# Kernel optimization log

Hardware: AMD Instinct MI355X
Metric: run time of the kernel (lower is better)

The kernel has to match this reference:

```python
import jax, jax.numpy as jnp
import numpy as np

N_NODES = 100000
N_EDGES = 1600000
N_PAIRS = 500000
K_HOPS = 6


def _bn(x, g, b, eps):
    # training-mode batch norm over the node/edge (batch) axis, biased variance
    mu = jnp.mean(x, axis=0)
    var = jnp.var(x, axis=0)
    return (x - mu) * jax.lax.rsqrt(var + eps) * g + b


def _gelu(x):
    return jax.nn.gelu(x, approximate=False)  # torch GELU default (erf)


def setup_inputs() -> dict:
    key = jax.random.key(0)
    ks = jax.random.split(key, 20)
    F, EF = 128, 32

    def w(k, shape, s=0.05):
        return jax.random.normal(k, shape, dtype=jnp.float32) * s

    return {
        'X': jax.random.normal(ks[0], (N_NODES, F), jnp.float32),
        'Y': jax.random.normal(ks[1], (N_PAIRS, EF), jnp.float32),
        'edge_index': jax.random.randint(ks[2], (2, N_EDGES), 0, N_NODES, jnp.int32),
        'inds0': jax.random.randint(ks[3], (N_PAIRS,), 0, N_NODES, jnp.int32),
        'inds1': jax.random.randint(ks[4], (N_PAIRS,), 0, N_NODES, jnp.int32),
        'bn_node_g': jnp.ones((F,), jnp.float32),
        'bn_node_b': jnp.zeros((F,), jnp.float32),
        'tag_lin_W': w(ks[5], (F, 128)),
        'tag_lin_b': jnp.zeros((128,), jnp.float32),
        'tag_Ws': w(ks[6], (K_HOPS + 1, 128, 128)),
        'tag_bias': jnp.zeros((128,), jnp.float32),
        'nl_W0': w(ks[7], (256, 256)),
        'nl_b0': jnp.zeros((256,), jnp.float32),
        'nl_W1': w(ks[8], (256, 128)),
        'nl_b1': jnp.zeros((128,), jnp.float32),
        'cl_W': w(ks[9], (128, 128)),
        'cl_b': jnp.zeros((128,), jnp.float32),
        'end_W': w(ks[10], (128, 8)),
        'end_b': jnp.zeros((8,), jnp.float32),
        'bn_edge_g': jnp.ones((544,), jnp.float32),
        'bn_edge_b': jnp.zeros((544,), jnp.float32),
        'el_W0': w(ks[11], (544, 512)),
        'el_b0': jnp.zeros((512,), jnp.float32),
        'el_W1': w(ks[12], (512, 256)),
        'el_b1': jnp.zeros((256,), jnp.float32),
        'el_end_W': w(ks[13], (256, 1)),
        'el_end_b': jnp.zeros((1,), jnp.float32),
    }


def reference(X, Y, bn_node_g, bn_node_b, tag_lin_W, tag_lin_b, tag_Ws, tag_bias,
              nl_W0, nl_b0, nl_W1, nl_b1, cl_W, cl_b, end_W, end_b,
              bn_edge_g, bn_edge_b, el_W0, el_b0, el_W1, el_b1, el_end_W, el_end_b,
              edge_index, inds0, inds1):
    N = X.shape[0]
    # ---- NodeGLAM ----
    x = _bn(X, bn_node_g, bn_node_b, 1e-5)
    # TagModule: Linear -> GELU -> TAGConv -> GELU
    h = _gelu(x @ tag_lin_W + tag_lin_b)
    src, dst = edge_index[0], edge_index[1]
    # gcn_norm (no self loops): deg over target, norm = d^-1/2[src]*d^-1/2[dst]
    deg = jax.ops.segment_sum(jnp.ones(src.shape, h.dtype), dst, num_segments=N)
    dinv = jnp.where(deg > 0, jax.lax.rsqrt(jnp.maximum(deg, 1.0)), 0.0)
    wgt = (dinv[src] * dinv[dst])[:, None]  # [E,1]
    out = h @ tag_Ws[0]
    hk = h
    for k in range(1, K_HOPS + 1):
        hk = jax.ops.segment_sum(hk[src] * wgt, dst, num_segments=N)  # gather-scale-scatter
        out = out + hk @ tag_Ws[k]
    h = _gelu(out + tag_bias)
    a = jnp.concatenate([x, h], axis=1)  # [N, 256]
    a = _gelu(a @ nl_W0 + nl_b0)
    a = _gelu(a @ nl_W1 + nl_b1)  # Node_embs [N,128]
    cl = _gelu(a @ cl_W + cl_b)
    node_classes = jax.nn.softmax(cl @ end_W + end_b, axis=-1)  # [N,8]
    # ---- edge feature gather + EdgeGLAM ----
    Omega = jnp.concatenate([a[inds0], a[inds1], X[inds0], X[inds1], Y], axis=1)  # [P,544]
    o = _bn(Omega, bn_edge_g, bn_edge_b, 1.0)  # BatchNorm(input_, output_) -> eps=1
    o = _gelu(o @ el_W0 + el_b0)
    o = _gelu(o @ el_W1 + el_b1)
    e_pred = jax.nn.sigmoid(o @ el_end_W + el_end_b)[:, 0]  # [P]
    return (node_classes, e_pred)
```

## Files before the change

kernel.cpp:

```cpp
#include <hip/hip_runtime.h>
#include <math.h>

#define NN 100000
#define NE 1600000
#define NP 500000
#define KHOPS 6
#define ECHK 50000
#define NB_SCAN ((NN + 1023) / 1024)

typedef unsigned short u16;
typedef short bf16x8 __attribute__((ext_vector_type(8)));
typedef float f32x4 __attribute__((ext_vector_type(4)));

__device__ __forceinline__ float gelu_erf(float x) {
    return 0.5f * x * (1.0f + erff(x * 0.70710678118654752f));
}
__device__ __forceinline__ float b2f(u16 u) {
    return __uint_as_float(((unsigned int)u) << 16);
}
__device__ __forceinline__ u16 f2b(float f) {
    unsigned int x = __float_as_uint(f);
    return (u16)((x + 0x7FFFu + ((x >> 16) & 1u)) >> 16);
}
__device__ __forceinline__ bf16x8 cvt8(float4 a, float4 b) {
    bf16x8 v;
    v[0]=(short)f2b(a.x); v[1]=(short)f2b(a.y); v[2]=(short)f2b(a.z); v[3]=(short)f2b(a.w);
    v[4]=(short)f2b(b.x); v[5]=(short)f2b(b.y); v[6]=(short)f2b(b.z); v[7]=(short)f2b(b.w);
    return v;
}

template<int BF>
__global__ void col_stats(const void* __restrict__ Matv, int rows, int lc,
                          const int* __restrict__ w0, const int* __restrict__ w1,
                          float* __restrict__ sums, float* __restrict__ sumsq,
                          int base0, int base1)
{
    __shared__ float red[256];
    const int t = threadIdx.x;
    const int C = 1 << lc;
    const long total = (long)rows << lc;
    const long stride = (long)gridDim.x * 256;
    float s0 = 0.f, q0 = 0.f, s1 = 0.f, q1 = 0.f;
    for (long idx = (long)blockIdx.x * 256 + t; idx < total; idx += stride) {
        int r = (int)(idx >> lc);
        float v = BF ? b2f(((const u16*)Matv)[idx]) : ((const float*)Matv)[idx];
        float f0 = w0 ? (float)w0[r] : 1.0f;
        s0 += f0 * v;
        q0 += f0 * v * v;
        if (w1) {
            float f1 = (float)w1[r];
            s1 += f1 * v;
            q1 += f1 * v * v;
        }
    }
    red[t] = s0; __syncthreads();
    if (t < C) { float x = 0.f; for (int k = t; k < 256; k += C) x += red[k]; atomicAdd(&sums[base0 + t], x); }
    __syncthreads();
    red[t] = q0; __syncthreads();
    if (t < C) { float x = 0.f; for (int k = t; k < 256; k += C) x += red[k]; atomicAdd(&sumsq[base0 + t], x); }
    __syncthreads();
    if (w1) {
        red[t] = s1; __syncthreads();
        if (t < C) { float x = 0.f; for (int k = t; k < 256; k += C) x += red[k]; atomicAdd(&sums[base1 + t], x); }
        __syncthreads();
        red[t] = q1; __syncthreads();
        if (t < C) { float x = 0.f; for (int k = t; k < 256; k += C) x += red[k]; atomicAdd(&sumsq[base1 + t], x); }
    }
}

__global__ void bn_finalize(const float* __restrict__ sums, const float* __restrict__ sumsq,
                            const float* __restrict__ g, const float* __restrict__ b,
                            float* __restrict__ s, float* __restrict__ t,
                            int C, float count, float eps)
{
    int c = blockIdx.x * blockDim.x + threadIdx.x;
    if (c < C) {
        float mu = sums[c] / count;
        float var = sumsq[c] / count - mu * mu;
        float sc = g[c] * rsqrtf(var + eps);
        s[c] = sc;
        t[c] = b[c] - mu * sc;
    }
}

__global__ void hist_add(const int* __restrict__ idx, int n, int* __restrict__ cnt)
{
    int stride = gridDim.x * blockDim.x;
    for (int i = blockIdx.x * blockDim.x + threadIdx.x; i < n; i += stride)
        atomicAdd(&cnt[idx[i]], 1);
}

__global__ void hist_add2(const int* __restrict__ i0, const int* __restrict__ i1, int n,
                          int* __restrict__ c0, int* __restrict__ c1)
{
    int stride = gridDim.x * blockDim.x;
    for (int i = blockIdx.x * blockDim.x + threadIdx.x; i < n; i += stride) {
        atomicAdd(&c0[i0[i]], 1);
        atomicAdd(&c1[i1[i]], 1);
    }
}

__global__ void scan1(const int* __restrict__ cnt, int* __restrict__ ex,
                      int* __restrict__ part, int n)
{
    __shared__ int buf[1024];
    int b = blockIdx.x, t = threadIdx.x;
    int i = b * 1024 + t;
    int v = (i < n) ? cnt[i] : 0;
    buf[t] = v;
    __syncthreads();
    int incl = v;
    for (int o = 1; o < 1024; o <<= 1) {
        int tmp = (t >= o) ? buf[t - o] : 0;
        __syncthreads();
        incl += tmp;
        buf[t] = incl;
        __syncthreads();
    }
    if (i < n) ex[i] = incl - v;
    if (t == 1023) part[b] = incl;
}

__global__ void scan2(int* __restrict__ part, int nb)
{
    __shared__ int s[256];
    int t = threadIdx.x;
    if (t < nb) s[t] = part[t];
    __syncthreads();
    if (t == 0) {
        int run = 0;
        for (int b = 0; b < nb; ++b) { int x = s[b]; part[b] = run; run += x; }
        part[nb] = run;
    }
}

__global__ void scan3(int* __restrict__ indptr, const int* __restrict__ part,
                      const int* __restrict__ cnt, float* __restrict__ dinv, int n)
{
    int b = blockIdx.x, t = threadIdx.x;
    int i = b * 1024 + t;
    if (i < n) {
        indptr[i] += part[b];
        int c = cnt[i];
        dinv[i] = (c > 0) ? rsqrtf((float)c) : 0.f;
    }
    if (b == 0 && t == 0) indptr[n] = part[NB_SCAN];
}

__global__ void csr_build(const int* __restrict__ src, const int* __restrict__ dst, int n,
                          const int* __restrict__ indptr, int* __restrict__ cursor,
                          int* __restrict__ csrS)
{
    int stride = gridDim.x * blockDim.x;
    for (int e = blockIdx.x * blockDim.x + threadIdx.x; e < n; e += stride) {
        int s = src[e], d = dst[e];
        int pos = indptr[d] + atomicAdd(&cursor[d], 1);
        csrS[pos] = s;
    }
}

__global__ void spmm_hop(const u16* __restrict__ hin, u16* __restrict__ hout,
                         const int* __restrict__ indptr, const int* __restrict__ csrS,
                         const float* __restrict__ dinv)
{
    int gid = blockIdx.x * blockDim.x + threadIdx.x;
    int node = gid >> 6;
    int lane = gid & 63;
    if (node >= NN) return;
    float dn = dinv[node];
    int beg = indptr[node], end = indptr[node + 1];
    float a0 = 0.f, a1 = 0.f;
    int e = beg;
    for (; e + 3 < end; e += 4) {
        int s0 = csrS[e], s1 = csrS[e + 1], s2 = csrS[e + 2], s3 = csrS[e + 3];
        float w0 = dn * dinv[s0], w1 = dn * dinv[s1];
        float w2 = dn * dinv[s2], w3 = dn * dinv[s3];
        ushort2 p0 = *(const ushort2*)(hin + (size_t)s0 * 128 + lane * 2);
        ushort2 p1 = *(const ushort2*)(hin + (size_t)s1 * 128 + lane * 2);
        ushort2 p2 = *(const ushort2*)(hin + (size_t)s2 * 128 + lane * 2);
        ushort2 p3 = *(const ushort2*)(hin + (size_t)s3 * 128 + lane * 2);
        a0 = fmaf(w0, b2f(p0.x), a0); a1 = fmaf(w0, b2f(p0.y), a1);
        a0 = fmaf(w1, b2f(p1.x), a0); a1 = fmaf(w1, b2f(p1.y), a1);
        a0 = fmaf(w2, b2f(p2.x), a0); a1 = fmaf(w2, b2f(p2.y), a1);
        a0 = fmaf(w3, b2f(p3.x), a0); a1 = fmaf(w3, b2f(p3.y), a1);
    }
    for (; e < end; ++e) {
        int s0 = csrS[e];
        float w0 = dn * dinv[s0];
        ushort2 p0 = *(const ushort2*)(hin + (size_t)s0 * 128 + lane * 2);
        a0 = fmaf(w0, b2f(p0.x), a0);
        a1 = fmaf(w0, b2f(p0.y), a1);
    }
    ushort2 o;
    o.x = f2b(a0); o.y = f2b(a1);
    *(ushort2*)(hout + (size_t)node * 128 + lane * 2) = o;
}

__global__ void convTB(const float* __restrict__ in, u16* __restrict__ out,
                       int K, int Nc, int B)
{
    int per = K * Nc;
    int i = blockIdx.x * blockDim.x + threadIdx.x;
    if (i < per * B) {
        int m = i / per, r = i - m * per;
        int n = r / K, k = r - n * K;
        out[i] = f2b(in[(size_t)m * per + (size_t)k * Nc + n]);
    }
}

__global__ void convB(const float* __restrict__ in, u16* __restrict__ out, int n4)
{
    int stride = gridDim.x * blockDim.x;
    for (int i = blockIdx.x * blockDim.x + threadIdx.x; i < n4; i += stride) {
        float4 v = ((const float4*)in)[i];
        ushort4 o;
        o.x = f2b(v.x); o.y = f2b(v.y); o.z = f2b(v.z); o.w = f2b(v.w);
        ((ushort4*)out)[i] = o;
    }
}

__global__ void fold_wT(const float* __restrict__ W0, const float* __restrict__ s,
                        u16* __restrict__ out)
{
    int i = blockIdx.x * blockDim.x + threadIdx.x;
    if (i < 512 * 544) {
        int n = i / 544, k = i - n * 544;
        out[i] = f2b(s[k] * W0[(size_t)k * 512 + n]);
    }
}

__global__ void fold_b(const float* __restrict__ W0, const float* __restrict__ b0,
                       const float* __restrict__ tv, float* __restrict__ bp)
{
    int j = blockIdx.x * blockDim.x + threadIdx.x;
    if (j < 512) {
        float s = b0[j];
        for (int k = 0; k < 544; ++k) s = fmaf(tv[k], W0[k * 512 + j], s);
        bp[j] = s;
    }
}

template<int AMODE>
__device__ __forceinline__ bf16x8 load_a_slot(
    const void* __restrict__ A0v, const void* __restrict__ A1v,
    const float* __restrict__ Yp, const int* __restrict__ i0s, const int* __restrict__ i1s,
    int rowOffset, const float* __restrict__ sv, const float* __restrict__ tv,
    int row, int r, int k0, int sl, int Mr, int lda)
{
    bf16x8 val = {0, 0, 0, 0, 0, 0, 0, 0};
    if (row < Mr) {
        if (AMODE == 0) {
            val = *(const bf16x8*)((const u16*)A0v + (size_t)row * lda + k0 + sl * 8);
        } else if (AMODE == 1) {
            int c = k0 + sl * 8;
            if (c < 128) {
                const float* xp = (const float*)A0v + (size_t)row * 128 + c;
                float4 x0 = *(const float4*)xp, x1 = *(const float4*)(xp + 4);
                float4 s0 = *(const float4*)(sv + c), s1 = *(const float4*)(sv + c + 4);
                float4 t0 = *(const float4*)(tv + c), t1 = *(const float4*)(tv + c + 4);
                float4 a = make_float4(fmaf(x0.x,s0.x,t0.x), fmaf(x0.y,s0.y,t0.y),
                                       fmaf(x0.z,s0.z,t0.z), fmaf(x0.w,s0.w,t0.w));
                float4 b = make_float4(fmaf(x1.x,s1.x,t1.x), fmaf(x1.y,s1.y,t1.y),
                                       fmaf(x1.z,s1.z,t1.z), fmaf(x1.w,s1.w,t1.w));
                val = cvt8(a, b);
            } else {
                val = *(const bf16x8*)((const u16*)A1v + (size_t)row * 128 + (c - 128));
            }
        } else if (AMODE == 3) {
            int c = k0 + sl * 8;
            const float* xp = (const float*)A0v + (size_t)row * 128 + c;
            float4 x0 = *(const float4*)xp, x1 = *(const float4*)(xp + 4);
            float4 s0 = *(const float4*)(sv + c), s1 = *(const float4*)(sv + c + 4);
            float4 t0 = *(const float4*)(tv + c), t1 = *(const float4*)(tv + c + 4);
            float4 a = make_float4(fmaf(x0.x,s0.x,t0.x), fmaf(x0.y,s0.y,t0.y),
                                   fmaf(x0.z,s0.z,t0.z), fmaf(x0.w,s0.w,t0.w));
            float4 b = make_float4(fmaf(x1.x,s1.x,t1.x), fmaf(x1.y,s1.y,t1.y),
                                   fmaf(x1.z,s1.z,t1.z), fmaf(x1.w,s1.w,t1.w));
            val = cvt8(a, b);
        } else {
            int seg = k0 >> 7;
            int c = (k0 & 127) + sl * 8;
            if (seg == 0) {
                val = *(const bf16x8*)((const u16*)A0v + (size_t)i0s[r] * 128 + c);
            } else if (seg == 1) {
                val = *(const bf16x8*)((const u16*)A0v + (size_t)i1s[r] * 128 + c);
            } else if (seg == 2) {
                val = *(const bf16x8*)((const u16*)A1v + (size_t)i0s[r] * 128 + c);
            } else if (seg == 3) {
                val = *(const bf16x8*)((const u16*)A1v + (size_t)i1s[r] * 128 + c);
            } else {
                const float* yp = Yp + (size_t)(rowOffset + row) * 32 + sl * 8;
                val = cvt8(*(const float4*)yp, *(const float4*)(yp + 4));
            }
        }
    }
    return val;
}

template<int AMODE, int ACT, int ACCUM, int OUTBF>
__launch_bounds__(256, 2)
__global__ void gemm_mfma(const void* __restrict__ A0v, const void* __restrict__ A1v,
                          const float* __restrict__ Yp,
                          const int* __restrict__ I0, const int* __restrict__ I1,
                          int rowOffset,
                          const float* __restrict__ sv, const float* __restrict__ tv,
                          const u16* __restrict__ Wb, const float* __restrict__ bias,
                          void* __restrict__ Cv, const float* __restrict__ Cacc,
                          int Mr, int Kd, int Nc, int lda)
{
    __shared__ __align__(16) u16 As[128 * 32];
    __shared__ __align__(16) u16 Bs[128 * 32];
    __shared__ int i0s[128], i1s[128];

    const int t = threadIdx.x;
    const int lane = t & 63;
    const int wid = t >> 6;
    const int wm = wid >> 1, wn = wid & 1;
    const int lb = lane & 15, lh = lane >> 4;
    const int row0 = blockIdx.x * 128;
    const int colb = blockIdx.y * 128;

    if (AMODE == 2) {
        if (t < 128) {
            int r = row0 + t;
            i0s[t] = (r < Mr) ? I0[rowOffset + r] : 0;
        } else {
            int r = row0 + (t - 128);
            i1s[t - 128] = (r < Mr) ? I1[rowOffset + r] : 0;
        }
    }

    f32x4 acc[4][4];
#pragma unroll
    for (int i = 0; i < 4; ++i)
#pragma unroll
        for (int j = 0; j < 4; ++j) acc[i][j] = (f32x4){0.f, 0.f, 0.f, 0.f};

    for (int k0 = 0; k0 < Kd; k0 += 32) {
        __syncthreads();
#pragma unroll
        for (int h = 0; h < 2; ++h) {
            int s = t + h * 256;
            int r = s >> 2, sl = s & 3;
            bf16x8 val = load_a_slot<AMODE>(A0v, A1v, Yp, i0s, i1s, rowOffset, sv, tv,
                                            row0 + r, r, k0, sl, Mr, lda);
            *(bf16x8*)&As[r * 32 + ((sl ^ ((r >> 1) & 3)) << 3)] = val;
        }
#pragma unroll
        for (int h = 0; h < 2; ++h) {
            int s = t + h * 256;
            int n = s >> 2, sl = s & 3;
            bf16x8 val = *(const bf16x8*)(Wb + (size_t)(colb + n) * Kd + k0 + sl * 8);
            *(bf16x8*)&Bs[n * 32 + ((sl ^ ((n >> 1) & 3)) << 3)] = val;
        }
        __syncthreads();
        bf16x8 af[4], bfr[4];
#pragma unroll
        for (int i = 0; i < 4; ++i) {
            int r = wm * 64 + i * 16 + lb;
            af[i] = *(const bf16x8*)&As[r * 32 + ((lh ^ ((r >> 1) & 3)) << 3)];
        }
#pragma unroll
        for (int j = 0; j < 4; ++j) {
            int n = wn * 64 + j * 16 + lb;
            bfr[j] = *(const bf16x8*)&Bs[n * 32 + ((lh ^ ((n >> 1) & 3)) << 3)];
        }
#pragma unroll
        for (int i = 0; i < 4; ++i)
#pragma unroll
            for (int j = 0; j < 4; ++j)
                acc[i][j] = __builtin_amdgcn_mfma_f32_16x16x32_bf16(af[i], bfr[j], acc[i][j], 0, 0, 0);
    }

#pragma unroll
    for (int i = 0; i < 4; ++i) {
#pragma unroll
        for (int j = 0; j < 4; ++j) {
            int col = colb + wn * 64 + j * 16 + lb;
#pragma unroll
            for (int r = 0; r < 4; ++r) {
                int row = row0 + wm * 64 + i * 16 + lh * 4 + r;
                if (row < Mr) {
                    size_t off = (size_t)row * Nc + col;
                    float v = acc[i][j][r];
                    if (ACCUM) v += Cacc[off];
                    if (ACT) v = gelu_erf(v + bias[col]);
                    if (OUTBF) ((u16*)Cv)[off] = f2b(v);
                    else       ((float*)Cv)[off] = v;
                }
            }
        }
    }
}

template<int AMODE, int ACT, int OUTBF>
__launch_bounds__(512, 4)
__global__ void gemm_wide(const void* __restrict__ A0v, const void* __restrict__ A1v,
                          const float* __restrict__ Yp,
                          const int* __restrict__ I0, const int* __restrict__ I1,
                          int rowOffset,
                          const float* __restrict__ sv, const float* __restrict__ tv,
                          const u16* __restrict__ Wb, const float* __restrict__ bias,
                          void* __restrict__ Cv, int Mr, int Kd, int Nc)
{
    __shared__ __align__(16) u16 As[128 * 32];
    __shared__ __align__(16) u16 Bs[256 * 32];
    __shared__ int i0s[128], i1s[128];

    const int t = threadIdx.x;
    const int lane = t & 63;
    const int wid = t >> 6;
    const int wm = wid >> 2, wn = wid & 3;
    const int lb = lane & 15, lh = lane >> 4;
    const int row0 = blockIdx.x * 128;
    const int colb = blockIdx.y * 256;

    if (AMODE == 2) {
        if (t < 128) {
            int r = row0 + t;
            i0s[t] = (r < Mr) ? I0[rowOffset + r] : 0;
        } else if (t < 256) {
            int r = row0 + (t - 128);
            i1s[t - 128] = (r < Mr) ? I1[rowOffset + r] : 0;
        }
    }

    f32x4 acc[4][4];
#pragma unroll
    for (int i = 0; i < 4; ++i)
#pragma unroll
        for (int j = 0; j < 4; ++j) acc[i][j] = (f32x4){0.f, 0.f, 0.f, 0.f};

    for (int k0 = 0; k0 < Kd; k0 += 32) {
        __syncthreads();
        {
            int r = t >> 2, sl = t & 3;
            bf16x8 val = load_a_slot<AMODE>(A0v, A1v, Yp, i0s, i1s, rowOffset, sv, tv,
                                            row0 + r, r, k0, sl, Mr, 0);
            *(bf16x8*)&As[r * 32 + ((sl ^ ((r >> 1) & 3)) << 3)] = val;
        }
#pragma unroll
        for (int h = 0; h < 2; ++h) {
            int s = t + h * 512;
            int n = s >> 2, sl = s & 3;
            bf16x8 val = *(const bf16x8*)(Wb + (size_t)(colb + n) * Kd + k0 + sl * 8);
            *(bf16x8*)&Bs[n * 32 + ((sl ^ ((n >> 1) & 3)) << 3)] = val;
        }
        __syncthreads();
        bf16x8 af[4], bfr[4];
#pragma unroll
        for (int i = 0; i < 4; ++i) {
            int r = wm * 64 + i * 16 + lb;
            af[i] = *(const bf16x8*)&As[r * 32 + ((lh ^ ((r >> 1) & 3)) << 3)];
        }
#pragma unroll
        for (int j = 0; j < 4; ++j) {
            int n = wn * 64 + j * 16 + lb;
            bfr[j] = *(const bf16x8*)&Bs[n * 32 + ((lh ^ ((n >> 1) & 3)) << 3)];
        }
#pragma unroll
        for (int i = 0; i < 4; ++i)
#pragma unroll
            for (int j = 0; j < 4; ++j)
                acc[i][j] = __builtin_amdgcn_mfma_f32_16x16x32_bf16(af[i], bfr[j], acc[i][j], 0, 0, 0);
    }

#pragma unroll
    for (int i = 0; i < 4; ++i) {
#pragma unroll
        for (int j = 0; j < 4; ++j) {
            int col = colb + wn * 64 + j * 16 + lb;
#pragma unroll
            for (int r = 0; r < 4; ++r) {
                int row = row0 + wm * 64 + i * 16 + lh * 4 + r;
                if (row < Mr) {
                    size_t off = (size_t)row * Nc + col;
                    float v = acc[i][j][r];
                    if (ACT) v = gelu_erf(v + bias[col]);
                    if (OUTBF) ((u16*)Cv)[off] = f2b(v);
                    else       ((float*)Cv)[off] = v;
                }
            }
        }
    }
}

__launch_bounds__(512, 4)
__global__ void gemm_head(const u16* __restrict__ A0, const u16* __restrict__ Wb,
                          const float* __restrict__ bias, const float* __restrict__ eW,
                          const float* __restrict__ eb,
                          float* __restrict__ outp, int outOffset, int Mr)
{
    __shared__ __align__(16) u16 As[128 * 32];
    __shared__ __align__(16) u16 Bs[256 * 32];
    __shared__ float bls[256], ews[256];
    __shared__ float sred[4][128];

    const int t = threadIdx.x;
    const int lane = t & 63;
    const int wid = t >> 6;
    const int wm = wid >> 2, wn = wid & 3;
    const int lb = lane & 15, lh = lane >> 4;
    const int row0 = blockIdx.x * 128;
    const int Kd = 512;

    if (t < 256) { bls[t] = bias[t]; ews[t] = eW[t]; }

    f32x4 acc[4][4];
#pragma unroll
    for (int i = 0; i < 4; ++i)
#pragma unroll
        for (int j = 0; j < 4; ++j) acc[i][j] = (f32x4){0.f, 0.f, 0.f, 0.f};

    for (int k0 = 0; k0 < Kd; k0 += 32) {
        __syncthreads();
        {
            int r = t >> 2, sl = t & 3;
            int row = row0 + r;
            bf16x8 val = {0,0,0,0,0,0,0,0};
            if (row < Mr) val = *(const bf16x8*)(A0 + (size_t)row * 512 + k0 + sl * 8);
            *(bf16x8*)&As[r * 32 + ((sl ^ ((r >> 1) & 3)) << 3)] = val;
        }
#pragma unroll
        for (int h = 0; h < 2; ++h) {
            int s = t + h * 512;
            int n = s >> 2, sl = s & 3;
            bf16x8 val = *(const bf16x8*)(Wb + (size_t)n * Kd + k0 + sl * 8);
            *(bf16x8*)&Bs[n * 32 + ((sl ^ ((n >> 1) & 3)) << 3)] = val;
        }
        __syncthreads();
        bf16x8 af[4], bfr[4];
#pragma unroll
        for (int i = 0; i < 4; ++i) {
            int r = wm * 64 + i * 16 + lb;
            af[i] = *(const bf16x8*)&As[r * 32 + ((lh ^ ((r >> 1) & 3)) << 3)];
        }
#pragma unroll
        for (int j = 0; j < 4; ++j) {
            int n = wn * 64 + j * 16 + lb;
            bfr[j] = *(const bf16x8*)&Bs[n * 32 + ((lh ^ ((n >> 1) & 3)) << 3)];
        }
#pragma unroll
        for (int i = 0; i < 4; ++i)
#pragma unroll
            for (int j = 0; j < 4; ++j)
                acc[i][j] = __builtin_amdgcn_mfma_f32_16x16x32_bf16(af[i], bfr[j], acc[i][j], 0, 0, 0);
    }

#pragma unroll
    for (int i = 0; i < 4; ++i) {
#pragma unroll
        for (int r = 0; r < 4; ++r) {
            float p = 0.f;
#pragma unroll
            for (int j = 0; j < 4; ++j) {
                int col = wn * 64 + j * 16 + lb;
                p += gelu_erf(acc[i][j][r] + bls[col]) * ews[col];
            }
            p += __shfl_xor(p, 1);
            p += __shfl_xor(p, 2);
            p += __shfl_xor(p, 4);
            p += __shfl_xor(p, 8);
            if (lb == 0) sred[wn][wm * 64 + i * 16 + lh * 4 + r] = p;
        }
    }
    __syncthreads();
    if (t < 128) {
        int row = row0 + t;
        if (row < Mr) {
            float s = sred[0][t] + sred[1][t] + sred[2][t] + sred[3][t] + eb[0];
            outp[outOffset + row] = 1.f / (1.f + expf(-s));
        }
    }
}

__global__ void node_head(const float* __restrict__ cl, const float* __restrict__ Wend,
                          const float* __restrict__ bend, float* __restrict__ out, int m)
{
    __shared__ float WsT[8 * 128];
    __shared__ float bs[8];
    int t = threadIdx.x;
    for (int i = t; i < 1024; i += 256) {
        int k = i >> 3, j = i & 7;
        WsT[j * 128 + k] = Wend[i];
    }
    if (t < 8) bs[t] = bend[t];
    __syncthreads();
    int gid = blockIdx.x * 256 + t;
    int wave = gid >> 6, lane = gid & 63;
    if (wave >= m) return;
    float v0 = cl[(size_t)wave * 128 + lane];
    float v1 = cl[(size_t)wave * 128 + lane + 64];
    float lg[8];
#pragma unroll
    for (int j = 0; j < 8; ++j) {
        float p = v0 * WsT[j * 128 + lane] + v1 * WsT[j * 128 + lane + 64];
#pragma unroll
        for (int o = 32; o; o >>= 1) p += __shfl_down(p, o);
        lg[j] = p;
    }
    if (lane == 0) {
        float mx = -1e30f;
#pragma unroll
        for (int j = 0; j < 8; ++j) { lg[j] += bs[j]; mx = fmaxf(mx, lg[j]); }
        float s = 0.f;
#pragma unroll
        for (int j = 0; j < 8; ++j) { lg[j] = expf(lg[j] - mx); s += lg[j]; }
        float inv = 1.f / s;
#pragma unroll
        for (int j = 0; j < 8; ++j) out[(size_t)wave * 8 + j] = lg[j] * inv;
    }
}

extern "C" void kernel_launch(void* const* d_in, const int* in_sizes, int n_in,
                              void* d_out, int out_size, void* d_ws, size_t ws_size,
                              hipStream_t stream)
{
    const float* X    = (const float*)d_in[0];
    const float* Y    = (const float*)d_in[1];
    const int*   EI   = (const int*)d_in[2];
    const int*   I0   = (const int*)d_in[3];
    const int*   I1   = (const int*)d_in[4];
    const float* bnG  = (const float*)d_in[5];
    const float* bnB  = (const float*)d_in[6];
    const float* Wlin = (const float*)d_in[7];
    const float* blin = (const float*)d_in[8];
    const float* tagWs= (const float*)d_in[9];
    const float* tagB = (const float*)d_in[10];
    const float* nlW0 = (const float*)d_in[11];
    const float* nlb0 = (const float*)d_in[12];
    const float* nlW1 = (const float*)d_in[13];
    const float* nlb1 = (const float*)d_in[14];
    const float* clW  = (const float*)d_in[15];
    const float* clb  = (const float*)d_in[16];
    const float* endW = (const float*)d_in[17];
    const float* endB = (const float*)d_in[18];
    const float* beG  = (const float*)d_in[19];
    const float* beB  = (const float*)d_in[20];
    const float* elW0 = (const float*)d_in[21];
    const float* elb0 = (const float*)d_in[22];
    const float* elW1 = (const float*)d_in[23];
    const float* elb1 = (const float*)d_in[24];
    const float* elEW = (const float*)d_in[25];
    const float* elEb = (const float*)d_in[26];

    const int N = NN, E = NE, P = NP;

    char* w = (char*)d_ws;
    size_t off = 0;
    auto alloc = [&](size_t bytes) -> void* {
        void* p = w + off;
        off += (bytes + 255) & ~(size_t)255;
        return p;
    };

    size_t zeroBytes = (size_t)(544 + 544 + 128 + 128) * 4 + (size_t)4 * N * 4;
    char* zr = (char*)alloc(zeroBytes);
    float* statS = (float*)zr;
    float* statQ = statS + 544;
    float* nodeS = statQ + 544;
    float* nodeQ = nodeS + 128;
    int* cnt    = (int*)(nodeQ + 128);
    int* cursor = cnt + N;
    int* cnt0   = cursor + N;
    int* cnt1   = cnt0 + N;

    int*   indptr = (int*)alloc((size_t)(N + 1) * 4);
    int*   part   = (int*)alloc((size_t)(NB_SCAN + 1) * 4);
    float* dinv   = (float*)alloc((size_t)N * 4);
    int*   csrS   = (int*)alloc((size_t)E * 4);
    float* sNode  = (float*)alloc(128 * 4);
    float* tNode  = (float*)alloc(128 * 4);
    float* sEdge  = (float*)alloc(544 * 4);
    float* tEdge  = (float*)alloc(544 * 4);
    float* b0p    = (float*)alloc(512 * 4);
    u16* Wlinb  = (u16*)alloc((size_t)128 * 128 * 2);
    u16* tagWsb = (u16*)alloc((size_t)7 * 128 * 128 * 2);
    u16* nlW0b  = (u16*)alloc((size_t)256 * 256 * 2);
    u16* nlW1b  = (u16*)alloc((size_t)128 * 256 * 2);
    u16* clWb   = (u16*)alloc((size_t)128 * 128 * 2);
    u16* elW1b  = (u16*)alloc((size_t)256 * 512 * 2);
    u16* W0pb   = (u16*)alloc((size_t)512 * 544 * 2);
    u16*   hA   = (u16*)alloc((size_t)N * 128 * 2);
    u16*   hB   = (u16*)alloc((size_t)N * 128 * 2);
    float* outT = (float*)alloc((size_t)N * 128 * 4);

    if (ws_size < off) return;

    u16*   aEmb  = hA;
    u16*   houtb = hB;
    float* out_nodes = (float*)d_out;
    float* out_epred = (float*)d_out + (size_t)N * 8;

    hipMemsetAsync(zr, 0, zeroBytes, stream);

    convTB<<<(128*128 + 255)/256, 256, 0, stream>>>(Wlin, Wlinb, 128, 128, 1);
    convTB<<<(7*128*128 + 255)/256, 256, 0, stream>>>(tagWs, tagWsb, 128, 128, 7);
    convTB<<<(256*256 + 255)/256, 256, 0, stream>>>(nlW0, nlW0b, 256, 256, 1);
    convTB<<<(256*128 + 255)/256, 256, 0, stream>>>(nlW1, nlW1b, 256, 128, 1);
    convTB<<<(128*128 + 255)/256, 256, 0, stream>>>(clW, clWb, 128, 128, 1);
    convTB<<<(512*256 + 255)/256, 256, 0, stream>>>(elW1, elW1b, 512, 256, 1);

    col_stats<0><<<1024, 256, 0, stream>>>(X, N, 7, nullptr, nullptr, nodeS, nodeQ, 0, 0);
    bn_finalize<<<1, 128, 0, stream>>>(nodeS, nodeQ, bnG, bnB, sNode, tNode, 128, (float)N, 1e-5f);

    dim3 g1((N + 127) / 128, 1);
    gemm_mfma<3, 1, 0, 1><<<g1, 256, 0, stream>>>(X, nullptr, nullptr, nullptr, nullptr, 0,
                                                  sNode, tNode, Wlinb, blin, hA, nullptr, N, 128, 128, 128);

    hist_add<<<2048, 256, 0, stream>>>(EI + E, E, cnt);
    hist_add2<<<1024, 256, 0, stream>>>(I0, I1, P, cnt0, cnt1);
    scan1<<<NB_SCAN, 1024, 0, stream>>>(cnt, indptr, part, N);
    scan2<<<1, 256, 0, stream>>>(part, NB_SCAN);
    scan3<<<NB_SCAN, 1024, 0, stream>>>(indptr, part, cnt, dinv, N);
    csr_build<<<2048, 256, 0, stream>>>(EI, EI + E, E, indptr, cursor, csrS);

    gemm_mfma<0, 0, 0, 0><<<g1, 256, 0, stream>>>(hA, nullptr, nullptr, nullptr, nullptr, 0,
                                                  nullptr, nullptr, tagWsb, nullptr, outT, nullptr,
                                                  N, 128, 128, 128);
    u16* cur = hA; u16* nxt = hB;
    for (int k = 1; k < KHOPS; ++k) {
        spmm_hop<<<(N * 64 + 255) / 256, 256, 0, stream>>>(cur, nxt, indptr, csrS, dinv);
        gemm_mfma<0, 0, 1, 0><<<g1, 256, 0, stream>>>(nxt, nullptr, nullptr, nullptr, nullptr, 0,
                                                      nullptr, nullptr, tagWsb + (size_t)k*128*128,
                                                      nullptr, outT, outT, N, 128, 128, 128);
        u16* tmp = cur; cur = nxt; nxt = tmp;
    }
    spmm_hop<<<(N * 64 + 255) / 256, 256, 0, stream>>>(cur, nxt, indptr, csrS, dinv);
    gemm_mfma<0, 1, 1, 1><<<g1, 256, 0, stream>>>(nxt, nullptr, nullptr, nullptr, nullptr, 0,
                                                  nullptr, nullptr, tagWsb + (size_t)KHOPS*128*128,
                                                  tagB, houtb, outT, N, 128, 128, 128);

    u16*   a256  = (u16*)outT;
    float* clbuf = outT;
    {
        dim3 gA((N + 127) / 128, 1);
        gemm_wide<1, 1, 1><<<gA, 512, 0, stream>>>(X, houtb, nullptr, nullptr, nullptr, 0,
                                                   sNode, tNode, nlW0b, nlb0, a256, N, 256, 256);
        dim3 gB((N + 127) / 128, 1);
        gemm_mfma<0, 1, 0, 1><<<gB, 256, 0, stream>>>(a256, nullptr, nullptr, nullptr, nullptr, 0,
                                                      nullptr, nullptr, nlW1b, nlb1, aEmb, nullptr,
                                                      N, 256, 128, 256);
        gemm_mfma<0, 1, 0, 0><<<gB, 256, 0, stream>>>(aEmb, nullptr, nullptr, nullptr, nullptr, 0,
                                                      nullptr, nullptr, clWb, clb, clbuf, nullptr,
                                                      N, 128, 128, 128);
        node_head<<<(N + 3) / 4, 256, 0, stream>>>(clbuf, endW, endB, out_nodes, N);
    }

    u16* Xb = hB;
    convB<<<2048, 256, 0, stream>>>(X, Xb, N * 128 / 4);

    col_stats<1><<<1024, 256, 0, stream>>>(aEmb, N, 7, cnt0, cnt1, statS, statQ, 0, 128);
    col_stats<1><<<1024, 256, 0, stream>>>(Xb,   N, 7, cnt0, cnt1, statS, statQ, 256, 384);
    col_stats<0><<<1024, 256, 0, stream>>>(Y,    P, 5, nullptr, nullptr, statS, statQ, 512, 0);
    bn_finalize<<<3, 256, 0, stream>>>(statS, statQ, beG, beB, sEdge, tEdge, 544, (float)P, 1.0f);
    fold_wT<<<(512*544 + 255)/256, 256, 0, stream>>>(elW0, sEdge, W0pb);
    fold_b<<<2, 256, 0, stream>>>(elW0, elb0, tEdge, b0p);

    u16* o1 = (u16*)outT;
    for (int pb = 0; pb < P; pb += ECHK) {
        int m = (P - pb < ECHK) ? (P - pb) : ECHK;
        dim3 gA((m + 127) / 128, 2);
        gemm_wide<2, 1, 1><<<gA, 512, 0, stream>>>(aEmb, Xb, Y, I0, I1, pb,
                                                   nullptr, nullptr, W0pb, b0p, o1, m, 544, 512);
        dim3 gB((m + 127) / 128, 1);
        gemm_head<<<gB, 512, 0, stream>>>(o1, elW1b, elb1, elEW, elEb, out_epred, pb, m);
    }
}
```

Baseline: 2.339 ms.

## Pair TAG hop GEMMs, unroll SpMM gather by 8, widen edge GEMM tile

New measurement: 4.848 ms. 2.07x slower.

```diff
diff --git a/kernel.cpp b/kernel.cpp
--- a/kernel.cpp
+++ b/kernel.cpp
@@ -171,18 +171,20 @@
     int beg = indptr[node], end = indptr[node + 1];
     float a0 = 0.f, a1 = 0.f;
     int e = beg;
-    for (; e + 3 < end; e += 4) {
-        int s0 = csrS[e], s1 = csrS[e + 1], s2 = csrS[e + 2], s3 = csrS[e + 3];
-        float w0 = dn * dinv[s0], w1 = dn * dinv[s1];
-        float w2 = dn * dinv[s2], w3 = dn * dinv[s3];
-        ushort2 p0 = *(const ushort2*)(hin + (size_t)s0 * 128 + lane * 2);
-        ushort2 p1 = *(const ushort2*)(hin + (size_t)s1 * 128 + lane * 2);
-        ushort2 p2 = *(const ushort2*)(hin + (size_t)s2 * 128 + lane * 2);
-        ushort2 p3 = *(const ushort2*)(hin + (size_t)s3 * 128 + lane * 2);
-        a0 = fmaf(w0, b2f(p0.x), a0); a1 = fmaf(w0, b2f(p0.y), a1);
-        a0 = fmaf(w1, b2f(p1.x), a0); a1 = fmaf(w1, b2f(p1.y), a1);
-        a0 = fmaf(w2, b2f(p2.x), a0); a1 = fmaf(w2, b2f(p2.y), a1);
-        a0 = fmaf(w3, b2f(p3.x), a0); a1 = fmaf(w3, b2f(p3.y), a1);
+    for (; e + 7 < end; e += 8) {
+        int sidx[8];
+        ushort2 pv[8];
+#pragma unroll
+        for (int u = 0; u < 8; ++u) sidx[u] = csrS[e + u];
+#pragma unroll
+        for (int u = 0; u < 8; ++u)
+            pv[u] = *(const ushort2*)(hin + (size_t)sidx[u] * 128 + lane * 2);
+#pragma unroll
+        for (int u = 0; u < 8; ++u) {
+            float wv = dn * dinv[sidx[u]];
+            a0 = fmaf(wv, b2f(pv[u].x), a0);
+            a1 = fmaf(wv, b2f(pv[u].y), a1);
+        }
     }
     for (; e < end; ++e) {
         int s0 = csrS[e];
@@ -208,6 +210,18 @@
     }
 }
 
+__global__ void conv_pair(const float* __restrict__ Ws, u16* __restrict__ out)
+{
+    int i = blockIdx.x * blockDim.x + threadIdx.x;
+    if (i < 3 * 128 * 256) {
+        int p = i >> 15;
+        int r = i & 32767;
+        int n = r >> 8, k = r & 255;
+        int hop = 2 * p + (k >> 7);
+        out[i] = f2b(Ws[(size_t)hop * 16384 + (size_t)(k & 127) * 128 + n]);
+    }
+}
+
 __global__ void convB(const float* __restrict__ in, u16* __restrict__ out, int n4)
 {
     int stride = gridDim.x * blockDim.x;
@@ -251,6 +265,10 @@
     if (row < Mr) {
         if (AMODE == 0) {
             val = *(const bf16x8*)((const u16*)A0v + (size_t)row * lda + k0 + sl * 8);
+        } else if (AMODE == 5) {
+            int c = k0 + sl * 8;
+            const u16* Ap = (c < 128) ? (const u16*)A0v : (const u16*)A1v;
+            val = *(const bf16x8*)(Ap + (size_t)row * 128 + (c & 127));
         } else if (AMODE == 1) {
             int c = k0 + sl * 8;
             if (c < 128) {
@@ -393,7 +411,7 @@
     }
 }
 
-template<int AMODE, int ACT, int OUTBF>
+template<int AMODE, int ACT, int OUTBF, int NCOLS>
 __launch_bounds__(512, 4)
 __global__ void gemm_wide(const void* __restrict__ A0v, const void* __restrict__ A1v,
                           const float* __restrict__ Yp,
@@ -403,8 +421,12 @@
                           const u16* __restrict__ Wb, const float* __restrict__ bias,
                           void* __restrict__ Cv, int Mr, int Kd, int Nc)
 {
+    constexpr int NJ = NCOLS / 64;
+    constexpr int WCOL = NCOLS / 4;
+    constexpr int BH = NCOLS / 128;
+
     __shared__ __align__(16) u16 As[128 * 32];
-    __shared__ __align__(16) u16 Bs[256 * 32];
+    __shared__ __align__(16) u16 Bs[NCOLS * 32];
     __shared__ int i0s[128], i1s[128];
 
     const int t = threadIdx.x;
@@ -413,7 +435,7 @@
     const int wm = wid >> 2, wn = wid & 3;
     const int lb = lane & 15, lh = lane >> 4;
     const int row0 = blockIdx.x * 128;
-    const int colb = blockIdx.y * 256;
+    const int colb = blockIdx.y * NCOLS;
 
     if (AMODE == 2) {
         if (t < 128) {
@@ -425,11 +447,11 @@
         }
     }
 
-    f32x4 acc[4][4];
+    f32x4 acc[4][NJ];
 #pragma unroll
     for (int i = 0; i < 4; ++i)
 #pragma unroll
-        for (int j = 0; j < 4; ++j) acc[i][j] = (f32x4){0.f, 0.f, 0.f, 0.f};
+        for (int j = 0; j < NJ; ++j) acc[i][j] = (f32x4){0.f, 0.f, 0.f, 0.f};
 
     for (int k0 = 0; k0 < Kd; k0 += 32) {
         __syncthreads();
@@ -440,36 +462,36 @@
             *(bf16x8*)&As[r * 32 + ((sl ^ ((r >> 1) & 3)) << 3)] = val;
         }
 #pragma unroll
-        for (int h = 0; h < 2; ++h) {
+        for (int h = 0; h < BH; ++h) {
             int s = t + h * 512;
             int n = s >> 2, sl = s & 3;
             bf16x8 val = *(const bf16x8*)(Wb + (size_t)(colb + n) * Kd + k0 + sl * 8);
             *(bf16x8*)&Bs[n * 32 + ((sl ^ ((n >> 1) & 3)) << 3)] = val;
         }
         __syncthreads();
-        bf16x8 af[4], bfr[4];
+        bf16x8 af[4], bfr[NJ];
 #pragma unroll
         for (int i = 0; i < 4; ++i) {
             int r = wm * 64 + i * 16 + lb;
             af[i] = *(const bf16x8*)&As[r * 32 + ((lh ^ ((r >> 1) & 3)) << 3)];
         }
 #pragma unroll
-        for (int j = 0; j < 4; ++j) {
-            int n = wn * 64 + j * 16 + lb;
+        for (int j = 0; j < NJ; ++j) {
+            int n = wn * WCOL + j * 16 + lb;
             bfr[j] = *(const bf16x8*)&Bs[n * 32 + ((lh ^ ((n >> 1) & 3)) << 3)];
         }
 #pragma unroll
         for (int i = 0; i < 4; ++i)
 #pragma unroll
-            for (int j = 0; j < 4; ++j)
+            for (int j = 0; j < NJ; ++j)
                 acc[i][j] = __builtin_amdgcn_mfma_f32_16x16x32_bf16(af[i], bfr[j], acc[i][j], 0, 0, 0);
     }
 
 #pragma unroll
     for (int i = 0; i < 4; ++i) {
 #pragma unroll
-        for (int j = 0; j < 4; ++j) {
-            int col = colb + wn * 64 + j * 16 + lb;
+        for (int j = 0; j < NJ; ++j) {
+            int col = colb + wn * WCOL + j * 16 + lb;
 #pragma unroll
             for (int r = 0; r < 4; ++r) {
                 int row = row0 + wm * 64 + i * 16 + lh * 4 + r;
@@ -675,7 +697,8 @@
     float* tEdge  = (float*)alloc(544 * 4);
     float* b0p    = (float*)alloc(512 * 4);
     u16* Wlinb  = (u16*)alloc((size_t)128 * 128 * 2);
-    u16* tagWsb = (u16*)alloc((size_t)7 * 128 * 128 * 2);
+    u16* tagWsPb= (u16*)alloc((size_t)3 * 128 * 256 * 2);
+    u16* tagW6b = (u16*)alloc((size_t)128 * 128 * 2);
     u16* nlW0b  = (u16*)alloc((size_t)256 * 256 * 2);
     u16* nlW1b  = (u16*)alloc((size_t)128 * 256 * 2);
     u16* clWb   = (u16*)alloc((size_t)128 * 128 * 2);
@@ -695,7 +718,8 @@
     hipMemsetAsync(zr, 0, zeroBytes, stream);
 
     convTB<<<(128*128 + 255)/256, 256, 0, stream>>>(Wlin, Wlinb, 128, 128, 1);
-    convTB<<<(7*128*128 + 255)/256, 256, 0, stream>>>(tagWs, tagWsb, 128, 128, 7);
+    conv_pair<<<(3*128*256 + 255)/256, 256, 0, stream>>>(tagWs, tagWsPb);
+    convTB<<<(128*128 + 255)/256, 256, 0, stream>>>(tagWs + (size_t)KHOPS*128*128, tagW6b, 128, 128, 1);
     convTB<<<(256*256 + 255)/256, 256, 0, stream>>>(nlW0, nlW0b, 256, 256, 1);
     convTB<<<(256*128 + 255)/256, 256, 0, stream>>>(nlW1, nlW1b, 256, 128, 1);
     convTB<<<(128*128 + 255)/256, 256, 0, stream>>>(clW, clWb, 128, 128, 1);
@@ -715,28 +739,32 @@
     scan3<<<NB_SCAN, 1024, 0, stream>>>(indptr, part, cnt, dinv, N);
     csr_build<<<2048, 256, 0, stream>>>(EI, EI + E, E, indptr, cursor, csrS);
 
-    gemm_mfma<0, 0, 0, 0><<<g1, 256, 0, stream>>>(hA, nullptr, nullptr, nullptr, nullptr, 0,
-                                                  nullptr, nullptr, tagWsb, nullptr, outT, nullptr,
+    int spmmGrid = (N * 64 + 255) / 256;
+    spmm_hop<<<spmmGrid, 256, 0, stream>>>(hA, hB, indptr, csrS, dinv);
+    gemm_mfma<5, 0, 0, 0><<<g1, 256, 0, stream>>>(hA, hB, nullptr, nullptr, nullptr, 0,
+                                                  nullptr, nullptr, tagWsPb, nullptr, outT, nullptr,
+                                                  N, 256, 128, 0);
+    spmm_hop<<<spmmGrid, 256, 0, stream>>>(hB, hA, indptr, csrS, dinv);
+    spmm_hop<<<spmmGrid, 256, 0, stream>>>(hA, hB, indptr, csrS, dinv);
+    gemm_mfma<5, 0, 1, 0><<<g1, 256, 0, stream>>>(hA, hB, nullptr, nullptr, nullptr, 0,
+                                                  nullptr, nullptr, tagWsPb + (size_t)1*128*256,
+                                                  nullptr, outT, outT, N, 256, 128, 0);
+    spmm_hop<<<spmmGrid, 256, 0, stream>>>(hB, hA, indptr, csrS, dinv);
+    spmm_hop<<<spmmGrid, 256, 0, stream>>>(hA, hB, indptr, csrS, dinv);
+    gemm_mfma<5, 0, 1, 0><<<g1, 256, 0, stream>>>(hA, hB, nullptr, nullptr, nullptr, 0,
+                                                  nullptr, nullptr, tagWsPb + (size_t)2*128*256,
+                                                  nullptr, outT, outT, N, 256, 128, 0);
+    spmm_hop<<<spmmGrid, 256, 0, stream>>>(hB, hA, indptr, csrS, dinv);
+    gemm_mfma<0, 1, 1, 1><<<g1, 256, 0, stream>>>(hA, nullptr, nullptr, nullptr, nullptr, 0,
+                                                  nullptr, nullptr, tagW6b, tagB, houtb, outT,
                                                   N, 128, 128, 128);
-    u16* cur = hA; u16* nxt = hB;
-    for (int k = 1; k < KHOPS; ++k) {
-        spmm_hop<<<(N * 64 + 255) / 256, 256, 0, stream>>>(cur, nxt, indptr, csrS, dinv);
-        gemm_mfma<0, 0, 1, 0><<<g1, 256, 0, stream>>>(nxt, nullptr, nullptr, nullptr, nullptr, 0,
-                                                      nullptr, nullptr, tagWsb + (size_t)k*128*128,
-                                                      nullptr, outT, outT, N, 128, 128, 128);
-        u16* tmp = cur; cur = nxt; nxt = tmp;
-    }
-    spmm_hop<<<(N * 64 + 255) / 256, 256, 0, stream>>>(cur, nxt, indptr, csrS, dinv);
-    gemm_mfma<0, 1, 1, 1><<<g1, 256, 0, stream>>>(nxt, nullptr, nullptr, nullptr, nullptr, 0,
-                                                  nullptr, nullptr, tagWsb + (size_t)KHOPS*128*128,
-                                                  tagB, houtb, outT, N, 128, 128, 128);
 
     u16*   a256  = (u16*)outT;
     float* clbuf = outT;
     {
         dim3 gA((N + 127) / 128, 1);
-        gemm_wide<1, 1, 1><<<gA, 512, 0, stream>>>(X, houtb, nullptr, nullptr, nullptr, 0,
-                                                   sNode, tNode, nlW0b, nlb0, a256, N, 256, 256);
+        gemm_wide<1, 1, 1, 256><<<gA, 512, 0, stream>>>(X, houtb, nullptr, nullptr, nullptr, 0,
+                                                        sNode, tNode, nlW0b, nlb0, a256, N, 256, 256);
         dim3 gB((N + 127) / 128, 1);
         gemm_mfma<0, 1, 0, 1><<<gB, 256, 0, stream>>>(a256, nullptr, nullptr, nullptr, nullptr, 0,
                                                       nullptr, nullptr, nlW1b, nlb1, aEmb, nullptr,
@@ -760,9 +788,9 @@
     u16* o1 = (u16*)outT;
     for (int pb = 0; pb < P; pb += ECHK) {
         int m = (P - pb < ECHK) ? (P - pb) : ECHK;
-        dim3 gA((m + 127) / 128, 2);
-        gemm_wide<2, 1, 1><<<gA, 512, 0, stream>>>(aEmb, Xb, Y, I0, I1, pb,
-                                                   nullptr, nullptr, W0pb, b0p, o1, m, 544, 512);
+        dim3 gA((m + 127) / 128, 1);
+        gemm_wide<2, 1, 1, 512><<<gA, 512, 0, stream>>>(aEmb, Xb, Y, I0, I1, pb,
+                                                        nullptr, nullptr, W0pb, b0p, o1, m, 544, 512);
         dim3 gB((m + 127) / 128, 1);
         gemm_head<<<gB, 512, 0, stream>>>(o1, elW1b, elb1, elEW, elEb, out_epred, pb, m);
     }
```
